# Performance work log

Hardware: AMD Instinct MI355X
Metric: run time of the kernel (lower is better)

The kernel has to match this reference:

```python
import jax, jax.numpy as jnp
import numpy as np

B, C_IN, L = 4, 512, 16384
C_RED = C_IN // 2  # q/k/v reduced channels = 256
BL = 64            # sliding-window block size
NEG = -jnp.inf


def setup_inputs() -> dict:
    key = jax.random.key(0)
    ks = jax.random.split(key, 8)
    x1 = jax.random.normal(ks[0], (B, C_IN, L), dtype=jnp.float32)
    x2 = jax.random.normal(ks[1], (B, C_IN, L), dtype=jnp.float32)
    mask = jnp.ones((B, 1, L), dtype=jnp.float32)
    s = 0.02
    Wq = jax.random.normal(ks[2], (C_RED, C_IN), dtype=jnp.float32) * s
    Wk = jax.random.normal(ks[3], (C_RED, C_IN), dtype=jnp.float32) * s
    Wv = jax.random.normal(ks[4], (C_RED, C_IN), dtype=jnp.float32) * s
    Wo = jax.random.normal(ks[5], (C_IN, C_RED), dtype=jnp.float32) * s
    bq = jnp.zeros((C_RED,), jnp.float32)
    bk = jnp.zeros((C_RED,), jnp.float32)
    bv = jnp.zeros((C_RED,), jnp.float32)
    bo = jnp.zeros((C_IN,), jnp.float32)
    return {"x1": x1, "x2": x2, "mask": mask, "Wq": Wq, "bq": bq,
            "Wk": Wk, "bk": bk, "Wv": Wv, "bv": bv, "Wo": Wo, "bo": bo}


def _conv1x1(W, b, x):
    # x: (B, Cin, L) -> (B, Cout, L)
    return jnp.einsum('oc,bcl->bol', W, x) + b[None, :, None]


def reference(x1, x2, mask, Wq, bq, Wk, bk, Wv, bv, Wo, bo):
    # encoder stage: value comes from x1 (x2 unused)
    q = _conv1x1(Wq, bq, x1)  # (B, C, L)
    k = _conv1x1(Wk, bk, x1)
    v = _conv1x1(Wv, bv, x1)

    Bq, C, Lq = q.shape
    bl = BL
    nb = (Lq + bl - 1) // bl
    pad = nb * bl - Lq
    if pad > 0:
        q = jnp.pad(q, ((0, 0), (0, 0), (0, pad)))
        k = jnp.pad(k, ((0, 0), (0, 0), (0, pad)))
        v = jnp.pad(v, ((0, 0), (0, 0), (0, pad)))
        mask = jnp.pad(mask, ((0, 0), (0, 0), (0, pad)))

    # non-overlapping windows: (B, C, nb, bl)
    qb = q.reshape(Bq, C, nb, bl)
    kb = k.reshape(Bq, C, nb, bl)
    vb = v.reshape(Bq, C, nb, bl)
    mb = mask.reshape(Bq, 1, nb, bl)  # (B,1,nb,bl)

    scale = 1.0 / jnp.sqrt(jnp.float32(C))
    # per-block attention scores: (B, nb, bl_i, bl_j)
    scores = jnp.einsum('bcni,bcnj->bnij', qb, kb) * scale
    key_mask = mb[:, 0, :, None, :]  # (B, nb, 1, bl_j)
    scores = jnp.where(key_mask == 0, NEG, scores)
    probs = jax.nn.softmax(scores, axis=-1)
    attn = jnp.einsum('bnij,bcnj->bcni', probs, vb)  # (B, C, nb, bl)

    h = jax.nn.relu(attn)
    out = jnp.einsum('oc,bcni->boni', Wo, h) + bo[None, :, None, None]
    out = out.reshape(Bq, Wo.shape[0], nb * bl)
    if pad > 0:
        out = out[:, :, :Lq]
    return out
```

## Files before the change

### kernel.cpp

```cpp
#include <hip/hip_runtime.h>
#include <hip/hip_fp16.h>
#include <stdint.h>

#define BB    4
#define CIN   512
#define CRED  256
#define LL    16384
#define NBLK  256
#define WELEM 131072

typedef _Float16 half8 __attribute__((ext_vector_type(8)));
typedef float    f32x4 __attribute__((ext_vector_type(4)));

#define XT_OFF 0
#define S_OFF  0
#define P_OFF  16384
#define H_OFF  24576
#define Q_OFF  65536
#define K_OFF  98304
#define V_OFF  131072
#define LDS_BYTES 163840

#define SWZ(row) (((row) & 7) << 4)

__global__ void convert_weights(const float* __restrict__ Wq,
                                const float* __restrict__ Wk,
                                const float* __restrict__ Wv,
                                const float* __restrict__ Wo,
                                _Float16* __restrict__ dst) {
    int i = blockIdx.x * blockDim.x + threadIdx.x;
    int m = i >> 17;
    int e = i & (WELEM - 1);
    const float* src = (m == 0) ? Wq : (m == 1) ? Wk : (m == 2) ? Wv : Wo;
    dst[(size_t)m * WELEM + e] = (_Float16)src[e];
}

__global__ __launch_bounds__(512, 2)
void att_fused(const float* __restrict__ x1, const float* __restrict__ mask,
               const _Float16* __restrict__ W,
               const float* __restrict__ bq, const float* __restrict__ bk,
               const float* __restrict__ bv, const float* __restrict__ bo,
               float* __restrict__ out) {
    extern __shared__ char lds[];
    const int tid  = threadIdx.x;
    const int wid  = tid >> 6;
    const int lane = tid & 63;
    const int l15  = lane & 15;
    const int l4   = lane >> 4;
    const int blk  = blockIdx.x;
    const int b    = blk >> 8;
    const int n    = blk & 255;

    const _Float16* Wq = W;
    const _Float16* Wk = W + WELEM;
    const _Float16* Wv = W + 2 * WELEM;
    const _Float16* Wo = W + 3 * WELEM;

    {
        const int p  = tid & 255;
        const int hs = tid >> 8;
        const float* r0 = x1 + ((size_t)b * CIN + 2 * p) * LL + n * 64;
        const float* r1 = r0 + LL;
        #pragma unroll
        for (int g8 = 0; g8 < 8; ++g8) {
            const int g = hs * 8 + g8;
            f32x4 a = *(const f32x4*)(r0 + 4 * g);
            f32x4 c = *(const f32x4*)(r1 + 4 * g);
            #pragma unroll
            for (int u = 0; u < 4; ++u) {
                const int j = 4 * g + u;
                union { _Float16 h[2]; uint32_t w; } pk;
                pk.h[0] = (_Float16)a[u];
                pk.h[1] = (_Float16)c[u];
                *(uint32_t*)(lds + XT_OFF + j * 1024 + ((4 * p) ^ SWZ(j))) = pk.w;
            }
        }
    }
    __syncthreads();

    {
        const int mb = wid * 32;
        f32x4 acc[3][2][4];
        #pragma unroll
        for (int p = 0; p < 3; ++p)
            #pragma unroll
            for (int m = 0; m < 2; ++m)
                #pragma unroll
                for (int nt = 0; nt < 4; ++nt) acc[p][m][nt] = (f32x4){0.f, 0.f, 0.f, 0.f};

        #pragma unroll 4
        for (int ks = 0; ks < 16; ++ks) {
            const int k0 = ks * 32;
            const int kb = 2 * (k0 + l4 * 8);
            half8 xb[4];
            #pragma unroll
            for (int nt = 0; nt < 4; ++nt) {
                const int j = nt * 16 + l15;
                xb[nt] = *(const half8*)(lds + XT_OFF + j * 1024 + (kb ^ SWZ(j)));
            }
            #pragma unroll
            for (int mt = 0; mt < 2; ++mt) {
                const size_t off = (size_t)(mb + mt * 16 + l15) * CIN + k0 + l4 * 8;
                half8 aq = *(const half8*)(Wq + off);
                half8 ak = *(const half8*)(Wk + off);
                half8 av = *(const half8*)(Wv + off);
                #pragma unroll
                for (int nt = 0; nt < 4; ++nt) {
                    acc[0][mt][nt] = __builtin_amdgcn_mfma_f32_16x16x32_f16(aq, xb[nt], acc[0][mt][nt], 0, 0, 0);
                    acc[1][mt][nt] = __builtin_amdgcn_mfma_f32_16x16x32_f16(ak, xb[nt], acc[1][mt][nt], 0, 0, 0);
                    acc[2][mt][nt] = __builtin_amdgcn_mfma_f32_16x16x32_f16(av, xb[nt], acc[2][mt][nt], 0, 0, 0);
                }
            }
        }
        #pragma unroll
        for (int mt = 0; mt < 2; ++mt) {
            #pragma unroll
            for (int ri = 0; ri < 4; ++ri) {
                const int c = mb + mt * 16 + l4 * 4 + ri;
                const float bqv = bq[c], bkv = bk[c], bvv = bv[c];
                #pragma unroll
                for (int nt = 0; nt < 4; ++nt) {
                    const int j = nt * 16 + l15;
                    *(_Float16*)(lds + Q_OFF + j * 512 + ((2 * c) ^ SWZ(j))) =
                        (_Float16)(acc[0][mt][nt][ri] + bqv);
                    *(_Float16*)(lds + K_OFF + j * 512 + ((2 * c) ^ SWZ(j))) =
                        (_Float16)(acc[1][mt][nt][ri] + bkv);
                    *(_Float16*)(lds + V_OFF + c * 128 + ((2 * j) ^ SWZ(c))) =
                        (_Float16)(acc[2][mt][nt][ri] + bvv);
                }
            }
        }
    }
    __syncthreads();

    {
        const int i0 = (wid & 3) * 16;
        const int j0 = (wid >> 2) * 32;
        f32x4 sa0 = (f32x4){0.f, 0.f, 0.f, 0.f};
        f32x4 sa1 = (f32x4){0.f, 0.f, 0.f, 0.f};
        #pragma unroll
        for (int ks = 0; ks < 8; ++ks) {
            const int kb = 2 * (ks * 32 + l4 * 8);
            const int iq = i0 + l15;
            const int ja = j0 + l15;
            const int jb = j0 + 16 + l15;
            half8 qa = *(const half8*)(lds + Q_OFF + iq * 512 + (kb ^ SWZ(iq)));
            half8 k0f = *(const half8*)(lds + K_OFF + ja * 512 + (kb ^ SWZ(ja)));
            half8 k1f = *(const half8*)(lds + K_OFF + jb * 512 + (kb ^ SWZ(jb)));
            sa0 = __builtin_amdgcn_mfma_f32_16x16x32_f16(qa, k0f, sa0, 0, 0, 0);
            sa1 = __builtin_amdgcn_mfma_f32_16x16x32_f16(qa, k1f, sa1, 0, 0, 0);
        }
        #pragma unroll
        for (int ri = 0; ri < 4; ++ri) {
            const int i = i0 + l4 * 4 + ri;
            *(float*)(lds + S_OFF + i * 256 + 4 * (j0 + l15))      = sa0[ri] * 0.0625f;
            *(float*)(lds + S_OFF + i * 256 + 4 * (j0 + 16 + l15)) = sa1[ri] * 0.0625f;
        }
    }
    __syncthreads();

    {
        const int r   = tid >> 3;
        const int sub = tid & 7;
        const float* mrow = mask + (size_t)b * LL + n * 64;
        f32x4 s0 = *(const f32x4*)(lds + S_OFF + r * 256 + sub * 32);
        f32x4 s1 = *(const f32x4*)(lds + S_OFF + r * 256 + sub * 32 + 16);
        f32x4 m0 = *(const f32x4*)(mrow + sub * 8);
        f32x4 m1 = *(const f32x4*)(mrow + sub * 8 + 4);
        float v[8];
        #pragma unroll
        for (int u = 0; u < 4; ++u) {
            v[u]     = (m0[u] == 0.f) ? -1e30f : s0[u];
            v[u + 4] = (m1[u] == 0.f) ? -1e30f : s1[u];
        }
        float mx = v[0];
        #pragma unroll
        for (int u = 1; u < 8; ++u) mx = fmaxf(mx, v[u]);
        mx = fmaxf(mx, __shfl_xor(mx, 1));
        mx = fmaxf(mx, __shfl_xor(mx, 2));
        mx = fmaxf(mx, __shfl_xor(mx, 4));
        float e[8], sum = 0.f;
        #pragma unroll
        for (int u = 0; u < 8; ++u) { e[u] = __expf(v[u] - mx); sum += e[u]; }
        sum += __shfl_xor(sum, 1);
        sum += __shfl_xor(sum, 2);
        sum += __shfl_xor(sum, 4);
        const float inv = 1.f / sum;
        union { _Float16 h[8]; half8 v8; } pk;
        #pragma unroll
        for (int u = 0; u < 8; ++u) pk.h[u] = (_Float16)(e[u] * inv);
        *(half8*)(lds + P_OFF + r * 128 + ((sub * 16) ^ SWZ(r))) = pk.v8;
    }
    __syncthreads();

    {
        const int cb = wid * 32;
        f32x4 pv[2][4];
        #pragma unroll
        for (int m = 0; m < 2; ++m)
            #pragma unroll
            for (int nt = 0; nt < 4; ++nt) pv[m][nt] = (f32x4){0.f, 0.f, 0.f, 0.f};
        #pragma unroll
        for (int ks = 0; ks < 2; ++ks) {
            const int kb = 2 * (ks * 32 + l4 * 8);
            half8 pb[4];
            #pragma unroll
            for (int nt = 0; nt < 4; ++nt) {
                const int i = nt * 16 + l15;
                pb[nt] = *(const half8*)(lds + P_OFF + i * 128 + (kb ^ SWZ(i)));
            }
            #pragma unroll
            for (int mt = 0; mt < 2; ++mt) {
                const int c = cb + mt * 16 + l15;
                half8 va = *(const half8*)(lds + V_OFF + c * 128 + (kb ^ SWZ(c)));
                #pragma unroll
                for (int nt = 0; nt < 4; ++nt)
                    pv[mt][nt] = __builtin_amdgcn_mfma_f32_16x16x32_f16(va, pb[nt], pv[mt][nt], 0, 0, 0);
            }
        }
        #pragma unroll
        for (int mt = 0; mt < 2; ++mt) {
            #pragma unroll
            for (int ri = 0; ri < 4; ++ri) {
                const int c = cb + mt * 16 + l4 * 4 + ri;
                #pragma unroll
                for (int nt = 0; nt < 4; ++nt) {
                    const int i = nt * 16 + l15;
                    *(_Float16*)(lds + H_OFF + i * 512 + ((2 * c) ^ SWZ(i))) =
                        (_Float16)fmaxf(pv[mt][nt][ri], 0.f);
                }
            }
        }
    }
    __syncthreads();

    {
        const int mb = wid * 64;
        f32x4 oa[4][4];
        #pragma unroll
        for (int m = 0; m < 4; ++m)
            #pragma unroll
            for (int nt = 0; nt < 4; ++nt) oa[m][nt] = (f32x4){0.f, 0.f, 0.f, 0.f};
        #pragma unroll 4
        for (int ks = 0; ks < 8; ++ks) {
            const int k0 = ks * 32;
            const int kb = 2 * (k0 + l4 * 8);
            half8 hb[4];
            #pragma unroll
            for (int nt = 0; nt < 4; ++nt) {
                const int i = nt * 16 + l15;
                hb[nt] = *(const half8*)(lds + H_OFF + i * 512 + (kb ^ SWZ(i)));
            }
            #pragma unroll
            for (int mt = 0; mt < 4; ++mt) {
                const size_t off = (size_t)(mb + mt * 16 + l15) * CRED + k0 + l4 * 8;
                half8 wa = *(const half8*)(Wo + off);
                #pragma unroll
                for (int nt = 0; nt < 4; ++nt)
                    oa[mt][nt] = __builtin_amdgcn_mfma_f32_16x16x32_f16(wa, hb[nt], oa[mt][nt], 0, 0, 0);
            }
        }
        #pragma unroll
        for (int mt = 0; mt < 4; ++mt) {
            #pragma unroll
            for (int ri = 0; ri < 4; ++ri) {
                const int o = mb + mt * 16 + l4 * 4 + ri;
                const float bov = bo[o];
                float* orow = out + ((size_t)b * CIN + o) * LL + n * 64;
                #pragma unroll
                for (int nt = 0; nt < 4; ++nt)
                    orow[nt * 16 + l15] = oa[mt][nt][ri] + bov;
            }
        }
    }
}

extern "C" void kernel_launch(void* const* d_in, const int* in_sizes, int n_in,
                              void* d_out, int out_size, void* d_ws, size_t ws_size,
                              hipStream_t stream) {
    const float* x1   = (const float*)d_in[0];
    const float* mask = (const float*)d_in[2];
    const float* Wq   = (const float*)d_in[3];
    const float* bq   = (const float*)d_in[4];
    const float* Wk   = (const float*)d_in[5];
    const float* bk   = (const float*)d_in[6];
    const float* Wv   = (const float*)d_in[7];
    const float* bv   = (const float*)d_in[8];
    const float* Wo   = (const float*)d_in[9];
    const float* bo   = (const float*)d_in[10];
    float* out = (float*)d_out;
    _Float16* wbuf = (_Float16*)d_ws;

    (void)hipFuncSetAttribute((const void*)att_fused,
                              hipFuncAttributeMaxDynamicSharedMemorySize, LDS_BYTES);

    convert_weights<<<2048, 256, 0, stream>>>(Wq, Wk, Wv, Wo, wbuf);
    att_fused<<<BB * NBLK, 512, LDS_BYTES, stream>>>(x1, mask, wbuf, bq, bk, bv, bo, out);
}
```

Before: 186.7 us.

## Make blocks persistent over batch and prefetch next x tile during attention

The grid shrinks from 1024 blocks to 256, and each block loops over the 4 batch entries for its window. The x1 tile for the next batch is loaded into registers during the QKV GEMM and written to LDS during the score and PV stages, so global load latency overlaps compute. S/P/H buffers move into the Q/K region so X can be refilled while they are in use. Q/K/H stores are packed into 64-bit writes and S gets a swizzle. In exchange, only 256 blocks run on a 256-CU part, about one block per CU, which leaves one of the two block slots per CU empty.

```diff
diff --git a/kernel.cpp b/kernel.cpp
--- a/kernel.cpp
+++ b/kernel.cpp
@@ -13,15 +13,15 @@
 typedef float    f32x4 __attribute__((ext_vector_type(4)));
 
 #define XT_OFF 0
-#define S_OFF  0
-#define P_OFF  16384
-#define H_OFF  24576
 #define Q_OFF  65536
 #define K_OFF  98304
+#define S_OFF  65536
+#define P_OFF  81920
+#define H_OFF  90112
 #define V_OFF  131072
 #define LDS_BYTES 163840
 
-#define SWZ(row) (((row) & 7) << 4)
+#define SWZ(r) (((r)&7)<<4)
 
 __global__ void convert_weights(const float* __restrict__ Wq,
                                 const float* __restrict__ Wk,
@@ -33,6 +33,31 @@
     int e = i & (WELEM - 1);
     const float* src = (m == 0) ? Wq : (m == 1) ? Wk : (m == 2) ? Wv : Wo;
     dst[(size_t)m * WELEM + e] = (_Float16)src[e];
+}
+
+__device__ __forceinline__ void x_issue(const float* __restrict__ xb, int half,
+                                        int rb, f32x4 rE[4], f32x4 rO[4]) {
+    #pragma unroll
+    for (int i = 0; i < 4; ++i) {
+        const int c = 2 * rb + 64 * (half * 4 + i);
+        rE[i] = *(const f32x4*)(xb + (size_t)c * LL);
+        rO[i] = *(const f32x4*)(xb + (size_t)(c + 1) * LL);
+    }
+}
+__device__ __forceinline__ void x_commit(char* lds, int half, int jx, int rb,
+                                         const f32x4 rE[4], const f32x4 rO[4]) {
+    #pragma unroll
+    for (int i = 0; i < 4; ++i) {
+        const int col = 4 * rb + 128 * (half * 4 + i);
+        #pragma unroll
+        for (int u = 0; u < 4; ++u) {
+            union { _Float16 h[2]; uint32_t w; } p;
+            p.h[0] = (_Float16)rE[i][u];
+            p.h[1] = (_Float16)rO[i][u];
+            const int j = 4 * jx + u;
+            *(uint32_t*)(lds + XT_OFF + j * 1024 + (col ^ SWZ(j))) = p.w;
+        }
+    }
 }
 
 __global__ __launch_bounds__(512, 2)
@@ -47,38 +72,30 @@
     const int lane = tid & 63;
     const int l15  = lane & 15;
     const int l4   = lane >> 4;
-    const int blk  = blockIdx.x;
-    const int b    = blk >> 8;
-    const int n    = blk & 255;
+    const int n    = blockIdx.x;
+    const int jx   = tid & 15;
+    const int rb   = tid >> 4;
 
     const _Float16* Wq = W;
     const _Float16* Wk = W + WELEM;
     const _Float16* Wv = W + 2 * WELEM;
     const _Float16* Wo = W + 3 * WELEM;
 
+    f32x4 rE0[4], rO0[4], rE1[4], rO1[4];
+
     {
-        const int p  = tid & 255;
-        const int hs = tid >> 8;
-        const float* r0 = x1 + ((size_t)b * CIN + 2 * p) * LL + n * 64;
-        const float* r1 = r0 + LL;
-        #pragma unroll
-        for (int g8 = 0; g8 < 8; ++g8) {
-            const int g = hs * 8 + g8;
-            f32x4 a = *(const f32x4*)(r0 + 4 * g);
-            f32x4 c = *(const f32x4*)(r1 + 4 * g);
-            #pragma unroll
-            for (int u = 0; u < 4; ++u) {
-                const int j = 4 * g + u;
-                union { _Float16 h[2]; uint32_t w; } pk;
-                pk.h[0] = (_Float16)a[u];
-                pk.h[1] = (_Float16)c[u];
-                *(uint32_t*)(lds + XT_OFF + j * 1024 + ((4 * p) ^ SWZ(j))) = pk.w;
-            }
-        }
+        const float* xb0 = x1 + (size_t)n * 64 + 4 * jx;
+        x_issue(xb0, 0, rb, rE0, rO0);
+        x_commit(lds, 0, jx, rb, rE0, rO0);
+        x_issue(xb0, 1, rb, rE0, rO0);
+        x_commit(lds, 1, jx, rb, rE0, rO0);
     }
     __syncthreads();
 
-    {
+    for (int t = 0; t < BB; ++t) {
+        const int b = t;
+        const float* xnext = x1 + ((size_t)(b + 1) * CIN) * LL + n * 64 + 4 * jx;
+
         const int mb = wid * 32;
         f32x4 acc[3][2][4];
         #pragma unroll
@@ -86,192 +103,212 @@
             #pragma unroll
             for (int m = 0; m < 2; ++m)
                 #pragma unroll
-                for (int nt = 0; nt < 4; ++nt) acc[p][m][nt] = (f32x4){0.f, 0.f, 0.f, 0.f};
-
-        #pragma unroll 4
-        for (int ks = 0; ks < 16; ++ks) {
-            const int k0 = ks * 32;
-            const int kb = 2 * (k0 + l4 * 8);
-            half8 xb[4];
+                for (int q = 0; q < 4; ++q) acc[p][m][q] = (f32x4){0.f, 0.f, 0.f, 0.f};
+
+        const _Float16* wqb = Wq + (size_t)(mb + l15) * CIN + l4 * 8;
+        const _Float16* wkb = Wk + (size_t)(mb + l15) * CIN + l4 * 8;
+        const _Float16* wvb = Wv + (size_t)(mb + l15) * CIN + l4 * 8;
+
+        #pragma unroll
+        for (int h = 0; h < 2; ++h) {
+            if (t < BB - 1) {
+                if (h == 0) x_issue(xnext, 0, rb, rE0, rO0);
+                else        x_issue(xnext, 1, rb, rE1, rO1);
+            }
+            #pragma unroll 4
+            for (int k8 = 0; k8 < 8; ++k8) {
+                const int ks = h * 8 + k8;
+                const int kb = ks * 64 + l4 * 16;
+                half8 xb[4];
+                #pragma unroll
+                for (int nt = 0; nt < 4; ++nt) {
+                    const int j = nt * 16 + l15;
+                    xb[nt] = *(const half8*)(lds + XT_OFF + j * 1024 + (kb ^ SWZ(j)));
+                }
+                #pragma unroll
+                for (int mt = 0; mt < 2; ++mt) {
+                    const int woff = mt * 16 * CIN + ks * 32;
+                    half8 aq = *(const half8*)(wqb + woff);
+                    half8 ak = *(const half8*)(wkb + woff);
+                    half8 av = *(const half8*)(wvb + woff);
+                    #pragma unroll
+                    for (int nt = 0; nt < 4; ++nt) {
+                        acc[0][mt][nt] = __builtin_amdgcn_mfma_f32_16x16x32_f16(aq, xb[nt], acc[0][mt][nt], 0, 0, 0);
+                        acc[1][mt][nt] = __builtin_amdgcn_mfma_f32_16x16x32_f16(ak, xb[nt], acc[1][mt][nt], 0, 0, 0);
+                        acc[2][mt][nt] = __builtin_amdgcn_mfma_f32_16x16x32_f16(av, xb[nt], acc[2][mt][nt], 0, 0, 0);
+                    }
+                }
+            }
+        }
+        #pragma unroll
+        for (int mt = 0; mt < 2; ++mt) {
+            const int c0 = mb + mt * 16 + l4 * 4;
+            f32x4 bqv = *(const f32x4*)(bq + c0);
+            f32x4 bkv = *(const f32x4*)(bk + c0);
+            f32x4 bvv = *(const f32x4*)(bv + c0);
             #pragma unroll
             for (int nt = 0; nt < 4; ++nt) {
                 const int j = nt * 16 + l15;
-                xb[nt] = *(const half8*)(lds + XT_OFF + j * 1024 + (kb ^ SWZ(j)));
-            }
-            #pragma unroll
-            for (int mt = 0; mt < 2; ++mt) {
-                const size_t off = (size_t)(mb + mt * 16 + l15) * CIN + k0 + l4 * 8;
-                half8 aq = *(const half8*)(Wq + off);
-                half8 ak = *(const half8*)(Wk + off);
-                half8 av = *(const half8*)(Wv + off);
-                #pragma unroll
-                for (int nt = 0; nt < 4; ++nt) {
-                    acc[0][mt][nt] = __builtin_amdgcn_mfma_f32_16x16x32_f16(aq, xb[nt], acc[0][mt][nt], 0, 0, 0);
-                    acc[1][mt][nt] = __builtin_amdgcn_mfma_f32_16x16x32_f16(ak, xb[nt], acc[1][mt][nt], 0, 0, 0);
-                    acc[2][mt][nt] = __builtin_amdgcn_mfma_f32_16x16x32_f16(av, xb[nt], acc[2][mt][nt], 0, 0, 0);
-                }
-            }
-        }
-        #pragma unroll
-        for (int mt = 0; mt < 2; ++mt) {
-            #pragma unroll
-            for (int ri = 0; ri < 4; ++ri) {
-                const int c = mb + mt * 16 + l4 * 4 + ri;
-                const float bqv = bq[c], bkv = bk[c], bvv = bv[c];
-                #pragma unroll
-                for (int nt = 0; nt < 4; ++nt) {
-                    const int j = nt * 16 + l15;
-                    *(_Float16*)(lds + Q_OFF + j * 512 + ((2 * c) ^ SWZ(j))) =
-                        (_Float16)(acc[0][mt][nt][ri] + bqv);
-                    *(_Float16*)(lds + K_OFF + j * 512 + ((2 * c) ^ SWZ(j))) =
-                        (_Float16)(acc[1][mt][nt][ri] + bkv);
+                union { _Float16 h[4]; uint64_t q; } qp, kp;
+                #pragma unroll
+                for (int ri = 0; ri < 4; ++ri) {
+                    qp.h[ri] = (_Float16)(acc[0][mt][nt][ri] + bqv[ri]);
+                    kp.h[ri] = (_Float16)(acc[1][mt][nt][ri] + bkv[ri]);
+                }
+                *(uint64_t*)(lds + Q_OFF + j * 512 + ((2 * c0) ^ SWZ(j))) = qp.q;
+                *(uint64_t*)(lds + K_OFF + j * 512 + ((2 * c0) ^ SWZ(j))) = kp.q;
+                #pragma unroll
+                for (int ri = 0; ri < 4; ++ri) {
+                    const int c = c0 + ri;
                     *(_Float16*)(lds + V_OFF + c * 128 + ((2 * j) ^ SWZ(c))) =
-                        (_Float16)(acc[2][mt][nt][ri] + bvv);
-                }
-            }
-        }
-    }
-    __syncthreads();
-
-    {
+                        (_Float16)(acc[2][mt][nt][ri] + bvv[ri]);
+                }
+            }
+        }
+        __syncthreads();
+
         const int i0 = (wid & 3) * 16;
         const int j0 = (wid >> 2) * 32;
         f32x4 sa0 = (f32x4){0.f, 0.f, 0.f, 0.f};
         f32x4 sa1 = (f32x4){0.f, 0.f, 0.f, 0.f};
         #pragma unroll
         for (int ks = 0; ks < 8; ++ks) {
-            const int kb = 2 * (ks * 32 + l4 * 8);
+            const int kb = ks * 64 + l4 * 16;
             const int iq = i0 + l15;
             const int ja = j0 + l15;
             const int jb = j0 + 16 + l15;
-            half8 qa = *(const half8*)(lds + Q_OFF + iq * 512 + (kb ^ SWZ(iq)));
+            half8 qa  = *(const half8*)(lds + Q_OFF + iq * 512 + (kb ^ SWZ(iq)));
             half8 k0f = *(const half8*)(lds + K_OFF + ja * 512 + (kb ^ SWZ(ja)));
             half8 k1f = *(const half8*)(lds + K_OFF + jb * 512 + (kb ^ SWZ(jb)));
             sa0 = __builtin_amdgcn_mfma_f32_16x16x32_f16(qa, k0f, sa0, 0, 0, 0);
             sa1 = __builtin_amdgcn_mfma_f32_16x16x32_f16(qa, k1f, sa1, 0, 0, 0);
         }
+        if (t < BB - 1) x_commit(lds, 0, jx, rb, rE0, rO0);
+        __syncthreads();
+
         #pragma unroll
         for (int ri = 0; ri < 4; ++ri) {
             const int i = i0 + l4 * 4 + ri;
-            *(float*)(lds + S_OFF + i * 256 + 4 * (j0 + l15))      = sa0[ri] * 0.0625f;
-            *(float*)(lds + S_OFF + i * 256 + 4 * (j0 + 16 + l15)) = sa1[ri] * 0.0625f;
-        }
-    }
-    __syncthreads();
-
-    {
-        const int r   = tid >> 3;
-        const int sub = tid & 7;
-        const float* mrow = mask + (size_t)b * LL + n * 64;
-        f32x4 s0 = *(const f32x4*)(lds + S_OFF + r * 256 + sub * 32);
-        f32x4 s1 = *(const f32x4*)(lds + S_OFF + r * 256 + sub * 32 + 16);
-        f32x4 m0 = *(const f32x4*)(mrow + sub * 8);
-        f32x4 m1 = *(const f32x4*)(mrow + sub * 8 + 4);
-        float v[8];
-        #pragma unroll
-        for (int u = 0; u < 4; ++u) {
-            v[u]     = (m0[u] == 0.f) ? -1e30f : s0[u];
-            v[u + 4] = (m1[u] == 0.f) ? -1e30f : s1[u];
-        }
-        float mx = v[0];
-        #pragma unroll
-        for (int u = 1; u < 8; ++u) mx = fmaxf(mx, v[u]);
-        mx = fmaxf(mx, __shfl_xor(mx, 1));
-        mx = fmaxf(mx, __shfl_xor(mx, 2));
-        mx = fmaxf(mx, __shfl_xor(mx, 4));
-        float e[8], sum = 0.f;
-        #pragma unroll
-        for (int u = 0; u < 8; ++u) { e[u] = __expf(v[u] - mx); sum += e[u]; }
-        sum += __shfl_xor(sum, 1);
-        sum += __shfl_xor(sum, 2);
-        sum += __shfl_xor(sum, 4);
-        const float inv = 1.f / sum;
-        union { _Float16 h[8]; half8 v8; } pk;
-        #pragma unroll
-        for (int u = 0; u < 8; ++u) pk.h[u] = (_Float16)(e[u] * inv);
-        *(half8*)(lds + P_OFF + r * 128 + ((sub * 16) ^ SWZ(r))) = pk.v8;
-    }
-    __syncthreads();
-
-    {
-        const int cb = wid * 32;
-        f32x4 pv[2][4];
-        #pragma unroll
-        for (int m = 0; m < 2; ++m)
-            #pragma unroll
-            for (int nt = 0; nt < 4; ++nt) pv[m][nt] = (f32x4){0.f, 0.f, 0.f, 0.f};
-        #pragma unroll
-        for (int ks = 0; ks < 2; ++ks) {
-            const int kb = 2 * (ks * 32 + l4 * 8);
-            half8 pb[4];
-            #pragma unroll
-            for (int nt = 0; nt < 4; ++nt) {
-                const int i = nt * 16 + l15;
-                pb[nt] = *(const half8*)(lds + P_OFF + i * 128 + (kb ^ SWZ(i)));
-            }
-            #pragma unroll
-            for (int mt = 0; mt < 2; ++mt) {
-                const int c = cb + mt * 16 + l15;
-                half8 va = *(const half8*)(lds + V_OFF + c * 128 + (kb ^ SWZ(c)));
-                #pragma unroll
-                for (int nt = 0; nt < 4; ++nt)
-                    pv[mt][nt] = __builtin_amdgcn_mfma_f32_16x16x32_f16(va, pb[nt], pv[mt][nt], 0, 0, 0);
-            }
-        }
-        #pragma unroll
-        for (int mt = 0; mt < 2; ++mt) {
-            #pragma unroll
-            for (int ri = 0; ri < 4; ++ri) {
-                const int c = cb + mt * 16 + l4 * 4 + ri;
+            *(float*)(lds + S_OFF + i * 256 + ((4 * (j0 + l15)) ^ SWZ(i)))      = sa0[ri] * 0.0625f;
+            *(float*)(lds + S_OFF + i * 256 + ((4 * (j0 + 16 + l15)) ^ SWZ(i))) = sa1[ri] * 0.0625f;
+        }
+        __syncthreads();
+
+        {
+            const int r   = tid >> 3;
+            const int sub = tid & 7;
+            const float* mrow = mask + (size_t)b * LL + n * 64;
+            f32x4 s0 = *(const f32x4*)(lds + S_OFF + r * 256 + ((sub * 32) ^ SWZ(r)));
+            f32x4 s1 = *(const f32x4*)(lds + S_OFF + r * 256 + ((sub * 32 + 16) ^ SWZ(r)));
+            f32x4 m0 = *(const f32x4*)(mrow + sub * 8);
+            f32x4 m1 = *(const f32x4*)(mrow + sub * 8 + 4);
+            float v[8];
+            #pragma unroll
+            for (int u = 0; u < 4; ++u) {
+                v[u]     = (m0[u] == 0.f) ? -1e30f : s0[u];
+                v[u + 4] = (m1[u] == 0.f) ? -1e30f : s1[u];
+            }
+            float mx = v[0];
+            #pragma unroll
+            for (int u = 1; u < 8; ++u) mx = fmaxf(mx, v[u]);
+            mx = fmaxf(mx, __shfl_xor(mx, 1));
+            mx = fmaxf(mx, __shfl_xor(mx, 2));
+            mx = fmaxf(mx, __shfl_xor(mx, 4));
+            float e[8], sum = 0.f;
+            #pragma unroll
+            for (int u = 0; u < 8; ++u) { e[u] = __expf(v[u] - mx); sum += e[u]; }
+            sum += __shfl_xor(sum, 1);
+            sum += __shfl_xor(sum, 2);
+            sum += __shfl_xor(sum, 4);
+            const float inv = 1.f / sum;
+            union { _Float16 h[8]; half8 v8; } pk;
+            #pragma unroll
+            for (int u = 0; u < 8; ++u) pk.h[u] = (_Float16)(e[u] * inv);
+            *(half8*)(lds + P_OFF + r * 128 + ((sub * 16) ^ SWZ(r))) = pk.v8;
+        }
+        __syncthreads();
+
+        {
+            const int cb = wid * 32;
+            f32x4 pv[2][4];
+            #pragma unroll
+            for (int m = 0; m < 2; ++m)
+                #pragma unroll
+                for (int q = 0; q < 4; ++q) pv[m][q] = (f32x4){0.f, 0.f, 0.f, 0.f};
+            #pragma unroll
+            for (int ks = 0; ks < 2; ++ks) {
+                const int kb = ks * 64 + l4 * 16;
+                half8 pb[4];
                 #pragma unroll
                 for (int nt = 0; nt < 4; ++nt) {
                     const int i = nt * 16 + l15;
-                    *(_Float16*)(lds + H_OFF + i * 512 + ((2 * c) ^ SWZ(i))) =
-                        (_Float16)fmaxf(pv[mt][nt][ri], 0.f);
-                }
-            }
-        }
-    }
-    __syncthreads();
-
-    {
-        const int mb = wid * 64;
-        f32x4 oa[4][4];
-        #pragma unroll
-        for (int m = 0; m < 4; ++m)
-            #pragma unroll
-            for (int nt = 0; nt < 4; ++nt) oa[m][nt] = (f32x4){0.f, 0.f, 0.f, 0.f};
-        #pragma unroll 4
-        for (int ks = 0; ks < 8; ++ks) {
-            const int k0 = ks * 32;
-            const int kb = 2 * (k0 + l4 * 8);
-            half8 hb[4];
-            #pragma unroll
-            for (int nt = 0; nt < 4; ++nt) {
-                const int i = nt * 16 + l15;
-                hb[nt] = *(const half8*)(lds + H_OFF + i * 512 + (kb ^ SWZ(i)));
+                    pb[nt] = *(const half8*)(lds + P_OFF + i * 128 + (kb ^ SWZ(i)));
+                }
+                #pragma unroll
+                for (int mt = 0; mt < 2; ++mt) {
+                    const int c = cb + mt * 16 + l15;
+                    half8 va = *(const half8*)(lds + V_OFF + c * 128 + (kb ^ SWZ(c)));
+                    #pragma unroll
+                    for (int nt = 0; nt < 4; ++nt)
+                        pv[mt][nt] = __builtin_amdgcn_mfma_f32_16x16x32_f16(va, pb[nt], pv[mt][nt], 0, 0, 0);
+                }
+            }
+            #pragma unroll
+            for (int mt = 0; mt < 2; ++mt) {
+                const int c0 = cb + mt * 16 + l4 * 4;
+                #pragma unroll
+                for (int nt = 0; nt < 4; ++nt) {
+                    const int j = nt * 16 + l15;
+                    union { _Float16 h[4]; uint64_t q; } hp;
+                    #pragma unroll
+                    for (int ri = 0; ri < 4; ++ri)
+                        hp.h[ri] = (_Float16)fmaxf(pv[mt][nt][ri], 0.f);
+                    *(uint64_t*)(lds + H_OFF + j * 512 + ((2 * c0) ^ SWZ(j))) = hp.q;
+                }
+            }
+            if (t < BB - 1) x_commit(lds, 1, jx, rb, rE1, rO1);
+        }
+        __syncthreads();
+
+        {
+            const int mbo = wid * 64;
+            const _Float16* wob = Wo + (size_t)(mbo + l15) * CRED + l4 * 8;
+            f32x4 oa[4][4];
+            #pragma unroll
+            for (int m = 0; m < 4; ++m)
+                #pragma unroll
+                for (int q = 0; q < 4; ++q) oa[m][q] = (f32x4){0.f, 0.f, 0.f, 0.f};
+            #pragma unroll 4
+            for (int ks = 0; ks < 8; ++ks) {
+                const int kb = ks * 64 + l4 * 16;
+                half8 hb[4];
+                #pragma unroll
+                for (int nt = 0; nt < 4; ++nt) {
+                    const int i = nt * 16 + l15;
+                    hb[nt] = *(const half8*)(lds + H_OFF + i * 512 + (kb ^ SWZ(i)));
+                }
+                #pragma unroll
+                for (int mt = 0; mt < 4; ++mt) {
+                    half8 wa = *(const half8*)(wob + mt * 16 * CRED + ks * 32);
+                    #pragma unroll
+                    for (int nt = 0; nt < 4; ++nt)
+                        oa[mt][nt] = __builtin_amdgcn_mfma_f32_16x16x32_f16(wa, hb[nt], oa[mt][nt], 0, 0, 0);
+                }
             }
             #pragma unroll
             for (int mt = 0; mt < 4; ++mt) {
-                const size_t off = (size_t)(mb + mt * 16 + l15) * CRED + k0 + l4 * 8;
-                half8 wa = *(const half8*)(Wo + off);
-                #pragma unroll
-                for (int nt = 0; nt < 4; ++nt)
-                    oa[mt][nt] = __builtin_amdgcn_mfma_f32_16x16x32_f16(wa, hb[nt], oa[mt][nt], 0, 0, 0);
-            }
-        }
-        #pragma unroll
-        for (int mt = 0; mt < 4; ++mt) {
-            #pragma unroll
-            for (int ri = 0; ri < 4; ++ri) {
-                const int o = mb + mt * 16 + l4 * 4 + ri;
-                const float bov = bo[o];
-                float* orow = out + ((size_t)b * CIN + o) * LL + n * 64;
-                #pragma unroll
-                for (int nt = 0; nt < 4; ++nt)
-                    orow[nt * 16 + l15] = oa[mt][nt][ri] + bov;
-            }
-        }
+                const int o0 = mbo + mt * 16 + l4 * 4;
+                f32x4 bov = *(const f32x4*)(bo + o0);
+                #pragma unroll
+                for (int ri = 0; ri < 4; ++ri) {
+                    float* orow = out + ((size_t)b * CIN + (o0 + ri)) * LL + n * 64;
+                    #pragma unroll
+                    for (int nt = 0; nt < 4; ++nt)
+                        orow[nt * 16 + l15] = oa[mt][nt][ri] + bov[ri];
+                }
+            }
+        }
+        __syncthreads();
     }
 }
 
@@ -295,5 +332,5 @@
                               hipFuncAttributeMaxDynamicSharedMemorySize, LDS_BYTES);
 
     convert_weights<<<2048, 256, 0, stream>>>(Wq, Wk, Wv, Wo, wbuf);
-    att_fused<<<BB * NBLK, 512, LDS_BYTES, stream>>>(x1, mask, wbuf, bq, bk, bv, bo, out);
-}
+    att_fused<<<NBLK, 512, LDS_BYTES, stream>>>(x1, mask, wbuf, bq, bk, bv, bo, out);
+}
```

Result: slower. 276.4 us (+48.0%).
